# Performance work log

Hardware: AMD Instinct MI355X
Metric: run time of the kernel (lower is better)

## Reference

```python
import jax, jax.numpy as jnp
import numpy as np

NUM_NODES = 100000
NUM_EDGES = 600000
NUM_GRAPHS = 1000
EMB = 128


def setup_inputs() -> dict:
    key = jax.random.key(0)
    ks = jax.random.split(key, 12)
    x = jax.random.normal(ks[0], (NUM_NODES, 4), dtype=jnp.float32)
    edge_index = jax.random.randint(ks[1], (2, NUM_EDGES), 0, NUM_NODES, dtype=jnp.int32)
    x_scalar = jax.random.normal(ks[2], (NUM_GRAPHS, 4), dtype=jnp.float32)
    batch_index = jnp.sort(jax.random.randint(ks[3], (NUM_NODES,), 0, NUM_GRAPHS, dtype=jnp.int32))
    def glorot(k, shape):
        fan_in, fan_out = shape[0], shape[1]
        s = jnp.sqrt(2.0 / (fan_in + fan_out)).astype(jnp.float32)
        return jax.random.normal(k, shape, dtype=jnp.float32) * s
    return {
        "x": x,
        "edge_index": edge_index,
        "x_scalar": x_scalar,
        "batch_index": batch_index,
        "W0": glorot(ks[4], (4, EMB)), "b0": jnp.zeros((EMB,), jnp.float32),
        "W1": glorot(ks[5], (EMB, EMB)), "b1": jnp.zeros((EMB,), jnp.float32),
        "W2": glorot(ks[6], (EMB, EMB)), "b2": jnp.zeros((EMB,), jnp.float32),
        "W3": glorot(ks[7], (EMB, EMB)), "b3": jnp.zeros((EMB,), jnp.float32),
        "Wl1": glorot(ks[8], (EMB + 4, 64)), "bl1": jnp.zeros((64,), jnp.float32),
        "Wl2": glorot(ks[9], (64, 1)), "bl2": jnp.zeros((1,), jnp.float32),
    }


def _gcn_norm(edge_index, num_nodes):
    # PyG GCNConv default: add self-loops, symmetric normalization
    loop = jnp.arange(num_nodes, dtype=edge_index.dtype)
    src = jnp.concatenate([edge_index[0], loop])
    dst = jnp.concatenate([edge_index[1], loop])
    deg = jax.ops.segment_sum(jnp.ones_like(src, dtype=jnp.float32), dst,
                              num_segments=num_nodes)
    dinv = jnp.where(deg > 0, jax.lax.rsqrt(jnp.maximum(deg, 1e-12)), 0.0)
    norm = dinv[src] * dinv[dst]  # [E+N]
    return src, dst, norm


def _gcn_conv(h, src, dst, norm, W, b, num_nodes):
    h = h @ W                                   # [N, out]
    msg = h[src] * norm[:, None]                # gather + normalize
    out = jax.ops.segment_sum(msg, dst, num_segments=num_nodes)  # scatter-add
    return out + b


def reference(x, edge_index, x_scalar, batch_index,
              W0, b0, W1, b1, W2, b2, W3, b3, Wl1, bl1, Wl2, bl2):
    n = x.shape[0]
    src, dst, norm = _gcn_norm(edge_index, n)
    h = jax.nn.relu(_gcn_conv(x, src, dst, norm, W0, b0, n))
    h = jax.nn.relu(_gcn_conv(h, src, dst, norm, W1, b1, n))
    h = jax.nn.relu(_gcn_conv(h, src, dst, norm, W2, b2, n))
    h = jax.nn.relu(_gcn_conv(h, src, dst, norm, W3, b3, n))
    # global mean pool over batch_index
    sums = jax.ops.segment_sum(h, batch_index, num_segments=NUM_GRAPHS)
    cnts = jax.ops.segment_sum(jnp.ones((n,), jnp.float32), batch_index,
                               num_segments=NUM_GRAPHS)
    pooled = sums / jnp.maximum(cnts, 1.0)[:, None]          # [G, EMB]
    feat = jnp.concatenate([pooled, x_scalar], axis=1)       # [G, EMB+4]
    out = jax.nn.relu(feat @ Wl1 + bl1) @ Wl2 + bl2          # [G, 1]
    return out
```

## Files before the change

### kernel.cpp

```cpp
#include <hip/hip_runtime.h>

#define NN 100000
#define EE 600000
#define GG 1000
#define NB ((NN + 255) / 256)
#define CAP 32
#define LDSPAD 136

typedef __bf16 bf16x8 __attribute__((ext_vector_type(8)));
typedef float f32x4 __attribute__((ext_vector_type(4)));
typedef unsigned int u32;

__device__ inline float2 bf2_to_f2(u32 u) {
  return make_float2(__uint_as_float(u << 16), __uint_as_float(u & 0xffff0000u));
}
__device__ inline u32 f2_to_bf2(float a, float b) {
  union { __bf16 h[2]; u32 u; } pk;
  pk.h[0] = (__bf16)a; pk.h[1] = (__bf16)b;
  return pk.u;
}


__global__ void k_init(int* cnt, int* gstart) {
  int i = blockIdx.x * 256 + threadIdx.x;
  if (i < NN) cnt[i] = 0;
  if (i <= GG) gstart[i] = NN;
}

__global__ void k_fill(const int* __restrict__ src, const int* __restrict__ dst,
                       int* cnt, int* __restrict__ ibucket) {
  int e = blockIdx.x * 256 + threadIdx.x;
  if (e >= EE) return;
  int s = src[e], d = dst[e];
  int pos = atomicAdd(&cnt[d], 1);
  if (pos < CAP - 1) ibucket[d * CAP + pos] = s;
}

__global__ void k_prep(const int* __restrict__ cnt, float* __restrict__ dinv,
                       const int* __restrict__ batch, int* gstart,
                       const float* __restrict__ W1, const float* __restrict__ W2,
                       const float* __restrict__ W3,
                       __bf16* __restrict__ Wt1, __bf16* __restrict__ Wt2,
                       __bf16* __restrict__ Wt3) {
  int gid = blockIdx.x * 256 + threadIdx.x;
  if (gid < NN) {
    dinv[gid] = rsqrtf((float)(cnt[gid] + 1));
    int b = batch[gid];
    if (gid == 0) {
      for (int g = 0; g <= b; ++g) gstart[g] = 0;
    } else {
      int prev = batch[gid - 1];
      for (int g = prev + 1; g <= b; ++g) gstart[g] = gid;
    }
  }
  if (gid < 3 * 16384) {
    int which = gid >> 14, idx = gid & 16383;
    int n = idx >> 7, k = idx & 127;
    const float* W = (which == 0) ? W1 : (which == 1) ? W2 : W3;
    __bf16* Wt = (which == 0) ? Wt1 : (which == 1) ? Wt2 : Wt3;
    Wt[(size_t)n * 128 + k] = (__bf16)W[(size_t)k * 128 + n];
  }
}

__global__ void k_wb(const int* __restrict__ ibucket, const int* __restrict__ cnt,
                     const float* __restrict__ dinv, int2* __restrict__ wbucket) {
  int gid = blockIdx.x * 256 + threadIdx.x;
  if (gid >= NN * CAP) return;
  int d = gid >> 5, slot = gid & 31;
  int m = min(cnt[d], CAP - 1);
  int mp = (m + 8) & ~7;
  if (slot >= mp) return;
  float dd = dinv[d];
  int s; float w;
  if (slot < m)      { s = ibucket[gid]; w = dinv[s] * dd; }
  else if (slot == m){ s = d;            w = dd * dd; }
  else               { s = d;            w = 0.f; }
  wbucket[gid] = make_int2(s, __float_as_int(w));
}


__global__ void k_aggx(const float4* __restrict__ x, const int* __restrict__ cnt,
                       const int2* __restrict__ wbucket, float4* __restrict__ y) {
  int i = blockIdx.x * 256 + threadIdx.x;
  if (i >= NN) return;
  int m1 = min(cnt[i], CAP - 1) + 1;
  float4 acc = make_float4(0.f, 0.f, 0.f, 0.f);
  for (int e = 0; e < m1; ++e) {
    int2 md = wbucket[i * CAP + e];
    float w = __int_as_float(md.y);
    float4 v = x[md.x];
    acc.x = fmaf(w, v.x, acc.x);
    acc.y = fmaf(w, v.y, acc.y);
    acc.z = fmaf(w, v.z, acc.z);
    acc.w = fmaf(w, v.w, acc.w);
  }
  y[i] = acc;
}


__global__ void k_lin0(const float4* __restrict__ y, const float* __restrict__ W0,
                       const float* __restrict__ b0, u32* __restrict__ hout2) {
  int gid = blockIdx.x * 256 + threadIdx.x;
  if (gid >= NN * 16) return;
  int node = gid >> 4, cg = gid & 15;
  float4 yv = y[node];
  float v[8];
  #pragma unroll
  for (int k = 0; k < 2; ++k) {
    float4 b = *(const float4*)(b0 + cg * 8 + k * 4);
    v[k * 4 + 0] = b.x; v[k * 4 + 1] = b.y; v[k * 4 + 2] = b.z; v[k * 4 + 3] = b.w;
  }
  #pragma unroll
  for (int k = 0; k < 4; ++k) {
    float yk = (k == 0) ? yv.x : (k == 1) ? yv.y : (k == 2) ? yv.z : yv.w;
    float4 wa = *(const float4*)(W0 + k * 128 + cg * 8);
    float4 wb = *(const float4*)(W0 + k * 128 + cg * 8 + 4);
    v[0] = fmaf(yk, wa.x, v[0]); v[1] = fmaf(yk, wa.y, v[1]);
    v[2] = fmaf(yk, wa.z, v[2]); v[3] = fmaf(yk, wa.w, v[3]);
    v[4] = fmaf(yk, wb.x, v[4]); v[5] = fmaf(yk, wb.y, v[5]);
    v[6] = fmaf(yk, wb.z, v[6]); v[7] = fmaf(yk, wb.w, v[7]);
  }
  uint4 o;
  o.x = f2_to_bf2(fmaxf(v[0], 0.f), fmaxf(v[1], 0.f));
  o.y = f2_to_bf2(fmaxf(v[2], 0.f), fmaxf(v[3], 0.f));
  o.z = f2_to_bf2(fmaxf(v[4], 0.f), fmaxf(v[5], 0.f));
  o.w = f2_to_bf2(fmaxf(v[6], 0.f), fmaxf(v[7], 0.f));
  *(uint4*)(hout2 + (size_t)node * 64 + cg * 4) = o;
}

__global__ __launch_bounds__(256) void k_agg23(const __bf16* __restrict__ hlin,
                                               const int* __restrict__ cnt,
                                               const int2* __restrict__ wbucket,
                                               u32* __restrict__ hout2) {
  int wid = (blockIdx.x * 4) + (threadIdx.x >> 6);
  int lane = threadIdx.x & 63;
  int ln = lane & 15, quad = lane >> 4;
  int na = wid * 2, nb = wid * 2 + 1;
  if (na >= NN) return;

  int nodeL = (lane < 32) ? na : nb;
  int2 me = make_int2(0, 0);
  if (nodeL < NN) me = wbucket[(size_t)nodeL * CAP + (lane & 31)];
  int s_l = me.x, w_l = me.y;
  int mpa = (min(cnt[na], CAP - 1) + 8) & ~7;
  int mpb = (nb < NN) ? ((min(cnt[nb], CAP - 1) + 8) & ~7) : 0;
  int mpmin = min(mpa, mpb);

  float aa[8] = {0.f, 0.f, 0.f, 0.f, 0.f, 0.f, 0.f, 0.f};
  float ab[8] = {0.f, 0.f, 0.f, 0.f, 0.f, 0.f, 0.f, 0.f};

  int j = 0;
  for (; j < mpmin; j += 8) {
    int p0 = (j + quad) * 4, p1 = (j + 4 + quad) * 4;
    int sa0 = __builtin_amdgcn_ds_bpermute(p0, s_l);
    int sa1 = __builtin_amdgcn_ds_bpermute(p1, s_l);
    int sb0 = __builtin_amdgcn_ds_bpermute(128 + p0, s_l);
    int sb1 = __builtin_amdgcn_ds_bpermute(128 + p1, s_l);
    float wa0 = __int_as_float(__builtin_amdgcn_ds_bpermute(p0, w_l));
    float wa1 = __int_as_float(__builtin_amdgcn_ds_bpermute(p1, w_l));
    float wb0 = __int_as_float(__builtin_amdgcn_ds_bpermute(128 + p0, w_l));
    float wb1 = __int_as_float(__builtin_amdgcn_ds_bpermute(128 + p1, w_l));
    uint4 ua0 = *(const uint4*)(hlin + ((size_t)sa0 << 7) + ln * 8);
    uint4 ua1 = *(const uint4*)(hlin + ((size_t)sa1 << 7) + ln * 8);
    uint4 ub0 = *(const uint4*)(hlin + ((size_t)sb0 << 7) + ln * 8);
    uint4 ub1 = *(const uint4*)(hlin + ((size_t)sb1 << 7) + ln * 8);
    float2 f;
    f = bf2_to_f2(ua0.x); aa[0] = fmaf(wa0, f.x, aa[0]); aa[1] = fmaf(wa0, f.y, aa[1]);
    f = bf2_to_f2(ua0.y); aa[2] = fmaf(wa0, f.x, aa[2]); aa[3] = fmaf(wa0, f.y, aa[3]);
    f = bf2_to_f2(ua0.z); aa[4] = fmaf(wa0, f.x, aa[4]); aa[5] = fmaf(wa0, f.y, aa[5]);
    f = bf2_to_f2(ua0.w); aa[6] = fmaf(wa0, f.x, aa[6]); aa[7] = fmaf(wa0, f.y, aa[7]);
    f = bf2_to_f2(ua1.x); aa[0] = fmaf(wa1, f.x, aa[0]); aa[1] = fmaf(wa1, f.y, aa[1]);
    f = bf2_to_f2(ua1.y); aa[2] = fmaf(wa1, f.x, aa[2]); aa[3] = fmaf(wa1, f.y, aa[3]);
    f = bf2_to_f2(ua1.z); aa[4] = fmaf(wa1, f.x, aa[4]); aa[5] = fmaf(wa1, f.y, aa[5]);
    f = bf2_to_f2(ua1.w); aa[6] = fmaf(wa1, f.x, aa[6]); aa[7] = fmaf(wa1, f.y, aa[7]);
    f = bf2_to_f2(ub0.x); ab[0] = fmaf(wb0, f.x, ab[0]); ab[1] = fmaf(wb0, f.y, ab[1]);
    f = bf2_to_f2(ub0.y); ab[2] = fmaf(wb0, f.x, ab[2]); ab[3] = fmaf(wb0, f.y, ab[3]);
    f = bf2_to_f2(ub0.z); ab[4] = fmaf(wb0, f.x, ab[4]); ab[5] = fmaf(wb0, f.y, ab[5]);
    f = bf2_to_f2(ub0.w); ab[6] = fmaf(wb0, f.x, ab[6]); ab[7] = fmaf(wb0, f.y, ab[7]);
    f = bf2_to_f2(ub1.x); ab[0] = fmaf(wb1, f.x, ab[0]); ab[1] = fmaf(wb1, f.y, ab[1]);
    f = bf2_to_f2(ub1.y); ab[2] = fmaf(wb1, f.x, ab[2]); ab[3] = fmaf(wb1, f.y, ab[3]);
    f = bf2_to_f2(ub1.z); ab[4] = fmaf(wb1, f.x, ab[4]); ab[5] = fmaf(wb1, f.y, ab[5]);
    f = bf2_to_f2(ub1.w); ab[6] = fmaf(wb1, f.x, ab[6]); ab[7] = fmaf(wb1, f.y, ab[7]);
  }
  for (; j < mpa; j += 8) {
    int p0 = (j + quad) * 4, p1 = (j + 4 + quad) * 4;
    int s0 = __builtin_amdgcn_ds_bpermute(p0, s_l);
    int s1 = __builtin_amdgcn_ds_bpermute(p1, s_l);
    float w0 = __int_as_float(__builtin_amdgcn_ds_bpermute(p0, w_l));
    float w1 = __int_as_float(__builtin_amdgcn_ds_bpermute(p1, w_l));
    uint4 u0 = *(const uint4*)(hlin + ((size_t)s0 << 7) + ln * 8);
    uint4 u1 = *(const uint4*)(hlin + ((size_t)s1 << 7) + ln * 8);
    float2 f;
    f = bf2_to_f2(u0.x); aa[0] = fmaf(w0, f.x, aa[0]); aa[1] = fmaf(w0, f.y, aa[1]);
    f = bf2_to_f2(u0.y); aa[2] = fmaf(w0, f.x, aa[2]); aa[3] = fmaf(w0, f.y, aa[3]);
    f = bf2_to_f2(u0.z); aa[4] = fmaf(w0, f.x, aa[4]); aa[5] = fmaf(w0, f.y, aa[5]);
    f = bf2_to_f2(u0.w); aa[6] = fmaf(w0, f.x, aa[6]); aa[7] = fmaf(w0, f.y, aa[7]);
    f = bf2_to_f2(u1.x); aa[0] = fmaf(w1, f.x, aa[0]); aa[1] = fmaf(w1, f.y, aa[1]);
    f = bf2_to_f2(u1.y); aa[2] = fmaf(w1, f.x, aa[2]); aa[3] = fmaf(w1, f.y, aa[3]);
    f = bf2_to_f2(u1.z); aa[4] = fmaf(w1, f.x, aa[4]); aa[5] = fmaf(w1, f.y, aa[5]);
    f = bf2_to_f2(u1.w); aa[6] = fmaf(w1, f.x, aa[6]); aa[7] = fmaf(w1, f.y, aa[7]);
  }
  for (; j < mpb; j += 8) {
    int p0 = 128 + (j + quad) * 4, p1 = 128 + (j + 4 + quad) * 4;
    int s0 = __builtin_amdgcn_ds_bpermute(p0, s_l);
    int s1 = __builtin_amdgcn_ds_bpermute(p1, s_l);
    float w0 = __int_as_float(__builtin_amdgcn_ds_bpermute(p0, w_l));
    float w1 = __int_as_float(__builtin_amdgcn_ds_bpermute(p1, w_l));
    uint4 u0 = *(const uint4*)(hlin + ((size_t)s0 << 7) + ln * 8);
    uint4 u1 = *(const uint4*)(hlin + ((size_t)s1 << 7) + ln * 8);
    float2 f;
    f = bf2_to_f2(u0.x); ab[0] = fmaf(w0, f.x, ab[0]); ab[1] = fmaf(w0, f.y, ab[1]);
    f = bf2_to_f2(u0.y); ab[2] = fmaf(w0, f.x, ab[2]); ab[3] = fmaf(w0, f.y, ab[3]);
    f = bf2_to_f2(u0.z); ab[4] = fmaf(w0, f.x, ab[4]); ab[5] = fmaf(w0, f.y, ab[5]);
    f = bf2_to_f2(u0.w); ab[6] = fmaf(w0, f.x, ab[6]); ab[7] = fmaf(w0, f.y, ab[7]);
    f = bf2_to_f2(u1.x); ab[0] = fmaf(w1, f.x, ab[0]); ab[1] = fmaf(w1, f.y, ab[1]);
    f = bf2_to_f2(u1.y); ab[2] = fmaf(w1, f.x, ab[2]); ab[3] = fmaf(w1, f.y, ab[3]);
    f = bf2_to_f2(u1.z); ab[4] = fmaf(w1, f.x, ab[4]); ab[5] = fmaf(w1, f.y, ab[5]);
    f = bf2_to_f2(u1.w); ab[6] = fmaf(w1, f.x, ab[6]); ab[7] = fmaf(w1, f.y, ab[7]);
  }

  #pragma unroll
  for (int k = 0; k < 8; ++k) {
    aa[k] += __shfl_xor(aa[k], 16); aa[k] += __shfl_xor(aa[k], 32);
    ab[k] += __shfl_xor(ab[k], 16); ab[k] += __shfl_xor(ab[k], 32);
  }
  if (quad == 0) {
    uint4 oa;
    oa.x = f2_to_bf2(aa[0], aa[1]); oa.y = f2_to_bf2(aa[2], aa[3]);
    oa.z = f2_to_bf2(aa[4], aa[5]); oa.w = f2_to_bf2(aa[6], aa[7]);
    *(uint4*)(hout2 + (size_t)na * 64 + ln * 4) = oa;
    if (nb < NN) {
      uint4 ob;
      ob.x = f2_to_bf2(ab[0], ab[1]); ob.y = f2_to_bf2(ab[2], ab[3]);
      ob.z = f2_to_bf2(ab[4], ab[5]); ob.w = f2_to_bf2(ab[6], ab[7]);
      *(uint4*)(hout2 + (size_t)nb * 64 + ln * 4) = ob;
    }
  }
}

__global__ __launch_bounds__(256) void k_mfma(const __bf16* __restrict__ hin,
                                              const __bf16* __restrict__ Wt,
                                              const float* __restrict__ bias,
                                              __bf16* __restrict__ hout) {
  __shared__ __bf16 As[128 * LDSPAD];
  int tid = threadIdx.x;
  int row0 = blockIdx.x * 128;
  int lane = tid & 63, w = tid >> 6;
  int ln = lane & 15, quad = lane >> 4;

  bf16x8 bfrag[8][4];
  float bcol[8];
  #pragma unroll
  for (int nt = 0; nt < 8; ++nt) {
    bcol[nt] = bias[nt * 16 + ln];
    #pragma unroll
    for (int kc = 0; kc < 4; ++kc)
      bfrag[nt][kc] = *(const bf16x8*)(Wt + (size_t)(nt * 16 + ln) * 128 + kc * 32 + quad * 8);
  }

  #pragma unroll
  for (int i = 0; i < 8; ++i) {
    int eb = (i * 256 + tid) * 8;
    int r = eb >> 7, c = eb & 127;
    int gr = row0 + r;
    uint4 v = make_uint4(0, 0, 0, 0);
    if (gr < NN) v = *(const uint4*)(hin + (size_t)gr * 128 + c);
    *(uint4*)&As[r * LDSPAD + c] = v;
  }
  __syncthreads();

  f32x4 acc[2][8];
  #pragma unroll
  for (int rt = 0; rt < 2; ++rt)
    #pragma unroll
    for (int nt = 0; nt < 8; ++nt) acc[rt][nt] = (f32x4){0.f, 0.f, 0.f, 0.f};

  #pragma unroll
  for (int kc = 0; kc < 4; ++kc) {
    bf16x8 a0 = *(const bf16x8*)&As[(w * 32 + ln) * LDSPAD + kc * 32 + quad * 8];
    bf16x8 a1 = *(const bf16x8*)&As[(w * 32 + 16 + ln) * LDSPAD + kc * 32 + quad * 8];
    #pragma unroll
    for (int nt = 0; nt < 8; ++nt) {
      acc[0][nt] = __builtin_amdgcn_mfma_f32_16x16x32_bf16(a0, bfrag[nt][kc], acc[0][nt], 0, 0, 0);
      acc[1][nt] = __builtin_amdgcn_mfma_f32_16x16x32_bf16(a1, bfrag[nt][kc], acc[1][nt], 0, 0, 0);
    }
  }

  #pragma unroll
  for (int rt = 0; rt < 2; ++rt)
    #pragma unroll
    for (int nt = 0; nt < 8; ++nt)
      #pragma unroll
      for (int reg = 0; reg < 4; ++reg) {
        int gr = row0 + w * 32 + rt * 16 + quad * 4 + reg;
        if (gr < NN)
          hout[(size_t)gr * 128 + nt * 16 + ln] =
              (__bf16)fmaxf(acc[rt][nt][reg] + bcol[nt], 0.f);
      }
}

__global__ __launch_bounds__(256) void k_poolmlp(const uint2* __restrict__ h4u,
                                                 const int* __restrict__ gstart,
                                                 const float* __restrict__ xs,
                                                 const float* __restrict__ Wl1,
                                                 const float* __restrict__ bl1,
                                                 const float* __restrict__ Wl2,
                                                 const float* __restrict__ bl2,
                                                 float* __restrict__ out) {
  __shared__ float4 part[8][32];
  __shared__ float pooled[128];
  int g = blockIdx.x;
  int beg = gstart[g], end = gstart[g + 1];
  int tid = threadIdx.x;
  int cg = tid & 31;
  int rg = tid >> 5;
  float4 acc = make_float4(0.f, 0.f, 0.f, 0.f);
  for (int i = beg + rg; i < end; i += 8) {
    uint2 u = h4u[(size_t)i * 32 + cg];
    acc.x += __uint_as_float(u.x << 16);
    acc.y += __uint_as_float(u.x & 0xffff0000u);
    acc.z += __uint_as_float(u.y << 16);
    acc.w += __uint_as_float(u.y & 0xffff0000u);
  }
  part[rg][cg] = acc;
  __syncthreads();
  if (tid < 32) {
    float4 s = part[0][tid];
    #pragma unroll
    for (int r = 1; r < 8; ++r) {
      float4 v = part[r][tid];
      s.x += v.x; s.y += v.y; s.z += v.z; s.w += v.w;
    }
    float sc = 1.f / fmaxf((float)(end - beg), 1.f);
    pooled[tid * 4 + 0] = s.x * sc;
    pooled[tid * 4 + 1] = s.y * sc;
    pooled[tid * 4 + 2] = s.z * sc;
    pooled[tid * 4 + 3] = s.w * sc;
  }
  __syncthreads();
  if (tid < 64) {
    float hj = bl1[tid];
    #pragma unroll 4
    for (int k = 0; k < 128; ++k) hj = fmaf(pooled[k], Wl1[k * 64 + tid], hj);
    const float* xr = xs + g * 4;
    #pragma unroll
    for (int k = 0; k < 4; ++k) hj = fmaf(xr[k], Wl1[(128 + k) * 64 + tid], hj);
    hj = fmaxf(hj, 0.f);
    float val = hj * Wl2[tid];
    #pragma unroll
    for (int off = 32; off > 0; off >>= 1) val += __shfl_down(val, off);
    if (tid == 0) out[g] = val + bl2[0];
  }
}


extern "C" void kernel_launch(void* const* d_in, const int* in_sizes, int n_in,
                              void* d_out, int out_size, void* d_ws, size_t ws_size,
                              hipStream_t stream) {
  const float* x    = (const float*)d_in[0];
  const int*   ei   = (const int*)d_in[1];
  const float* xs   = (const float*)d_in[2];
  const int*   batch= (const int*)d_in[3];
  const float* W0   = (const float*)d_in[4];
  const float* b0   = (const float*)d_in[5];
  const float* W1   = (const float*)d_in[6];
  const float* b1   = (const float*)d_in[7];
  const float* W2   = (const float*)d_in[8];
  const float* b2   = (const float*)d_in[9];
  const float* W3   = (const float*)d_in[10];
  const float* b3   = (const float*)d_in[11];
  const float* Wl1  = (const float*)d_in[12];
  const float* bl1  = (const float*)d_in[13];
  const float* Wl2  = (const float*)d_in[14];
  const float* bl2  = (const float*)d_in[15];
  const int* srcA = ei;
  const int* dstA = ei + EE;
  float* out = (float*)d_out;

  char* p = (char*)d_ws;
  auto take = [&](size_t bytes) { char* q = p; p += (bytes + 255) & ~(size_t)255; return q; };
  __bf16* hA    = (__bf16*)take((size_t)NN * 128 * 2);
  __bf16* hB    = (__bf16*)take((size_t)NN * 128 * 2);
  float*  y     = (float*)take((size_t)NN * 4 * 4);
  int*    cnt   = (int*)take((size_t)NN * 4);
  float*  dinv  = (float*)take((size_t)NN * 4);
  int*    ibucket = (int*)take((size_t)NN * CAP * 4);
  int2*   wbucket = (int2*)take((size_t)NN * CAP * 8);
  int*    gstart= (int*)take((size_t)(GG + 1) * 4);
  __bf16* Wt1   = (__bf16*)take(16384 * 2);
  __bf16* Wt2   = (__bf16*)take(16384 * 2);
  __bf16* Wt3   = (__bf16*)take(16384 * 2);

  k_init<<<NB, 256, 0, stream>>>(cnt, gstart);
  k_fill<<<(EE + 255) / 256, 256, 0, stream>>>(srcA, dstA, cnt, ibucket);
  k_prep<<<NB, 256, 0, stream>>>(cnt, dinv, batch, gstart, W1, W2, W3, Wt1, Wt2, Wt3);
  k_wb<<<(NN * CAP + 255) / 256, 256, 0, stream>>>(ibucket, cnt, dinv, wbucket);

  k_aggx<<<NB, 256, 0, stream>>>((const float4*)x, cnt, wbucket, (float4*)y);
  k_lin0<<<(NN * 16 + 255) / 256, 256, 0, stream>>>((const float4*)y, W0, b0, (u32*)hA);
  k_agg23<<<(NN + 7) / 8, 256, 0, stream>>>(hA, cnt, wbucket, (u32*)hB);
  k_mfma<<<(NN + 127) / 128, 256, 0, stream>>>(hB, Wt1, b1, hA);
  k_agg23<<<(NN + 7) / 8, 256, 0, stream>>>(hA, cnt, wbucket, (u32*)hB);
  k_mfma<<<(NN + 127) / 128, 256, 0, stream>>>(hB, Wt2, b2, hA);
  k_agg23<<<(NN + 7) / 8, 256, 0, stream>>>(hA, cnt, wbucket, (u32*)hB);
  k_mfma<<<(NN + 127) / 128, 256, 0, stream>>>(hB, Wt3, b3, hA);

  k_poolmlp<<<GG, 256, 0, stream>>>((const uint2*)hA, gstart, xs, Wl1, bl1, Wl2, bl2, out);
}
```

Before: 350.5 us.

## Fuse layer-0 aggregation into linear kernel and drop LDS staging in MFMA GEMM

```diff
diff --git a/kernel.cpp b/kernel.cpp
--- a/kernel.cpp
+++ b/kernel.cpp
@@ -5,7 +5,6 @@
 #define GG 1000
 #define NB ((NN + 255) / 256)
 #define CAP 32
-#define LDSPAD 136
 
 typedef __bf16 bf16x8 __attribute__((ext_vector_type(8)));
 typedef float f32x4 __attribute__((ext_vector_type(4)));
@@ -78,32 +77,24 @@
   wbucket[gid] = make_int2(s, __float_as_int(w));
 }
 
-
-__global__ void k_aggx(const float4* __restrict__ x, const int* __restrict__ cnt,
-                       const int2* __restrict__ wbucket, float4* __restrict__ y) {
-  int i = blockIdx.x * 256 + threadIdx.x;
-  if (i >= NN) return;
-  int m1 = min(cnt[i], CAP - 1) + 1;
-  float4 acc = make_float4(0.f, 0.f, 0.f, 0.f);
-  for (int e = 0; e < m1; ++e) {
-    int2 md = wbucket[i * CAP + e];
-    float w = __int_as_float(md.y);
-    float4 v = x[md.x];
-    acc.x = fmaf(w, v.x, acc.x);
-    acc.y = fmaf(w, v.y, acc.y);
-    acc.z = fmaf(w, v.z, acc.z);
-    acc.w = fmaf(w, v.w, acc.w);
-  }
-  y[i] = acc;
-}
-
-
-__global__ void k_lin0(const float4* __restrict__ y, const float* __restrict__ W0,
-                       const float* __restrict__ b0, u32* __restrict__ hout2) {
+__global__ void k_l0(const float4* __restrict__ x, const int* __restrict__ cnt,
+                     const int2* __restrict__ wbucket,
+                     const float* __restrict__ W0, const float* __restrict__ b0,
+                     u32* __restrict__ hout2) {
   int gid = blockIdx.x * 256 + threadIdx.x;
   if (gid >= NN * 16) return;
   int node = gid >> 4, cg = gid & 15;
-  float4 yv = y[node];
+  int m1 = min(cnt[node], CAP - 1) + 1;
+  float4 yv = make_float4(0.f, 0.f, 0.f, 0.f);
+  for (int e = 0; e < m1; ++e) {
+    int2 md = wbucket[(size_t)node * CAP + e];
+    float wgt = __int_as_float(md.y);
+    float4 v = x[md.x];
+    yv.x = fmaf(wgt, v.x, yv.x);
+    yv.y = fmaf(wgt, v.y, yv.y);
+    yv.z = fmaf(wgt, v.z, yv.z);
+    yv.w = fmaf(wgt, v.w, yv.w);
+  }
   float v[8];
   #pragma unroll
   for (int k = 0; k < 2; ++k) {
@@ -242,32 +233,29 @@
                                               const __bf16* __restrict__ Wt,
                                               const float* __restrict__ bias,
                                               __bf16* __restrict__ hout) {
-  __shared__ __bf16 As[128 * LDSPAD];
   int tid = threadIdx.x;
   int row0 = blockIdx.x * 128;
   int lane = tid & 63, w = tid >> 6;
   int ln = lane & 15, quad = lane >> 4;
 
-  bf16x8 bfrag[8][4];
   float bcol[8];
   #pragma unroll
-  for (int nt = 0; nt < 8; ++nt) {
-    bcol[nt] = bias[nt * 16 + ln];
-    #pragma unroll
-    for (int kc = 0; kc < 4; ++kc)
-      bfrag[nt][kc] = *(const bf16x8*)(Wt + (size_t)(nt * 16 + ln) * 128 + kc * 32 + quad * 8);
-  }
-
-  #pragma unroll
-  for (int i = 0; i < 8; ++i) {
-    int eb = (i * 256 + tid) * 8;
-    int r = eb >> 7, c = eb & 127;
-    int gr = row0 + r;
-    uint4 v = make_uint4(0, 0, 0, 0);
-    if (gr < NN) v = *(const uint4*)(hin + (size_t)gr * 128 + c);
-    *(uint4*)&As[r * LDSPAD + c] = v;
-  }
-  __syncthreads();
+  for (int nt = 0; nt < 8; ++nt) bcol[nt] = bias[nt * 16 + ln];
+
+  int r0 = row0 + w * 32 + ln;
+  int r1 = r0 + 16;
+  bf16x8 zero8;
+  #pragma unroll
+  for (int i = 0; i < 8; ++i) zero8[i] = (__bf16)0.f;
+
+  bf16x8 a0[4], a1[4];
+  #pragma unroll
+  for (int kc = 0; kc < 4; ++kc) {
+    a0[kc] = (r0 < NN) ? *(const bf16x8*)(hin + (size_t)r0 * 128 + kc * 32 + quad * 8)
+                       : zero8;
+    a1[kc] = (r1 < NN) ? *(const bf16x8*)(hin + (size_t)r1 * 128 + kc * 32 + quad * 8)
+                       : zero8;
+  }
 
   f32x4 acc[2][8];
   #pragma unroll
@@ -277,12 +265,11 @@
 
   #pragma unroll
   for (int kc = 0; kc < 4; ++kc) {
-    bf16x8 a0 = *(const bf16x8*)&As[(w * 32 + ln) * LDSPAD + kc * 32 + quad * 8];
-    bf16x8 a1 = *(const bf16x8*)&As[(w * 32 + 16 + ln) * LDSPAD + kc * 32 + quad * 8];
     #pragma unroll
     for (int nt = 0; nt < 8; ++nt) {
-      acc[0][nt] = __builtin_amdgcn_mfma_f32_16x16x32_bf16(a0, bfrag[nt][kc], acc[0][nt], 0, 0, 0);
-      acc[1][nt] = __builtin_amdgcn_mfma_f32_16x16x32_bf16(a1, bfrag[nt][kc], acc[1][nt], 0, 0, 0);
+      bf16x8 bf = *(const bf16x8*)(Wt + (size_t)(nt * 16 + ln) * 128 + kc * 32 + quad * 8);
+      acc[0][nt] = __builtin_amdgcn_mfma_f32_16x16x32_bf16(a0[kc], bf, acc[0][nt], 0, 0, 0);
+      acc[1][nt] = __builtin_amdgcn_mfma_f32_16x16x32_bf16(a1[kc], bf, acc[1][nt], 0, 0, 0);
     }
   }
 
@@ -381,7 +368,6 @@
   auto take = [&](size_t bytes) { char* q = p; p += (bytes + 255) & ~(size_t)255; return q; };
   __bf16* hA    = (__bf16*)take((size_t)NN * 128 * 2);
   __bf16* hB    = (__bf16*)take((size_t)NN * 128 * 2);
-  float*  y     = (float*)take((size_t)NN * 4 * 4);
   int*    cnt   = (int*)take((size_t)NN * 4);
   float*  dinv  = (float*)take((size_t)NN * 4);
   int*    ibucket = (int*)take((size_t)NN * CAP * 4);
@@ -396,8 +382,7 @@
   k_prep<<<NB, 256, 0, stream>>>(cnt, dinv, batch, gstart, W1, W2, W3, Wt1, Wt2, Wt3);
   k_wb<<<(NN * CAP + 255) / 256, 256, 0, stream>>>(ibucket, cnt, dinv, wbucket);
 
-  k_aggx<<<NB, 256, 0, stream>>>((const float4*)x, cnt, wbucket, (float4*)y);
-  k_lin0<<<(NN * 16 + 255) / 256, 256, 0, stream>>>((const float4*)y, W0, b0, (u32*)hA);
+  k_l0<<<(NN * 16 + 255) / 256, 256, 0, stream>>>((const float4*)x, cnt, wbucket, W0, b0, (u32*)hA);
   k_agg23<<<(NN + 7) / 8, 256, 0, stream>>>(hA, cnt, wbucket, (u32*)hB);
   k_mfma<<<(NN + 127) / 128, 256, 0, stream>>>(hB, Wt1, b1, hA);
   k_agg23<<<(NN + 7) / 8, 256, 0, stream>>>(hA, cnt, wbucket, (u32*)hB);
```

Result: no change. 354.8 us (+1.2%).

## Fuse layer-0 aggregate into linear, drop ibucket, pad edge lists to four

Applied to the files above, without the earlier changes.

```diff
diff --git a/kernel.cpp b/kernel.cpp
--- a/kernel.cpp
+++ b/kernel.cpp
@@ -28,12 +28,12 @@
 }
 
 __global__ void k_fill(const int* __restrict__ src, const int* __restrict__ dst,
-                       int* cnt, int* __restrict__ ibucket) {
+                       int* cnt, int2* __restrict__ wbucket) {
   int e = blockIdx.x * 256 + threadIdx.x;
   if (e >= EE) return;
   int s = src[e], d = dst[e];
   int pos = atomicAdd(&cnt[d], 1);
-  if (pos < CAP - 1) ibucket[d * CAP + pos] = s;
+  if (pos < CAP - 1) wbucket[d * CAP + pos].x = s;
 }
 
 __global__ void k_prep(const int* __restrict__ cnt, float* __restrict__ dinv,
@@ -62,48 +62,40 @@
   }
 }
 
-__global__ void k_wb(const int* __restrict__ ibucket, const int* __restrict__ cnt,
-                     const float* __restrict__ dinv, int2* __restrict__ wbucket) {
+__global__ void k_wb(const int* __restrict__ cnt, const float* __restrict__ dinv,
+                     int2* __restrict__ wbucket) {
   int gid = blockIdx.x * 256 + threadIdx.x;
   if (gid >= NN * CAP) return;
   int d = gid >> 5, slot = gid & 31;
   int m = min(cnt[d], CAP - 1);
-  int mp = (m + 8) & ~7;
+  int mp = (m + 4) & ~3;
   if (slot >= mp) return;
   float dd = dinv[d];
   int s; float w;
-  if (slot < m)      { s = ibucket[gid]; w = dinv[s] * dd; }
-  else if (slot == m){ s = d;            w = dd * dd; }
-  else               { s = d;            w = 0.f; }
+  if (slot < m)      { s = wbucket[gid].x; w = dinv[s] * dd; }
+  else if (slot == m){ s = d;              w = dd * dd; }
+  else               { s = d;              w = 0.f; }
   wbucket[gid] = make_int2(s, __float_as_int(w));
 }
 
-
-__global__ void k_aggx(const float4* __restrict__ x, const int* __restrict__ cnt,
-                       const int2* __restrict__ wbucket, float4* __restrict__ y) {
-  int i = blockIdx.x * 256 + threadIdx.x;
-  if (i >= NN) return;
-  int m1 = min(cnt[i], CAP - 1) + 1;
-  float4 acc = make_float4(0.f, 0.f, 0.f, 0.f);
-  for (int e = 0; e < m1; ++e) {
-    int2 md = wbucket[i * CAP + e];
-    float w = __int_as_float(md.y);
-    float4 v = x[md.x];
-    acc.x = fmaf(w, v.x, acc.x);
-    acc.y = fmaf(w, v.y, acc.y);
-    acc.z = fmaf(w, v.z, acc.z);
-    acc.w = fmaf(w, v.w, acc.w);
-  }
-  y[i] = acc;
-}
-
-
-__global__ void k_lin0(const float4* __restrict__ y, const float* __restrict__ W0,
-                       const float* __restrict__ b0, u32* __restrict__ hout2) {
+__global__ void k_l0(const float4* __restrict__ x, const int* __restrict__ cnt,
+                     const int2* __restrict__ wbucket,
+                     const float* __restrict__ W0, const float* __restrict__ b0,
+                     u32* __restrict__ hout2) {
   int gid = blockIdx.x * 256 + threadIdx.x;
   if (gid >= NN * 16) return;
   int node = gid >> 4, cg = gid & 15;
-  float4 yv = y[node];
+  int m1 = min(cnt[node], CAP - 1) + 1;
+  float4 yv = make_float4(0.f, 0.f, 0.f, 0.f);
+  for (int e = 0; e < m1; ++e) {
+    int2 md = wbucket[(size_t)node * CAP + e];
+    float wgt = __int_as_float(md.y);
+    float4 v = x[md.x];
+    yv.x = fmaf(wgt, v.x, yv.x);
+    yv.y = fmaf(wgt, v.y, yv.y);
+    yv.z = fmaf(wgt, v.z, yv.z);
+    yv.w = fmaf(wgt, v.w, yv.w);
+  }
   float v[8];
   #pragma unroll
   for (int k = 0; k < 2; ++k) {
@@ -142,15 +134,15 @@
   int2 me = make_int2(0, 0);
   if (nodeL < NN) me = wbucket[(size_t)nodeL * CAP + (lane & 31)];
   int s_l = me.x, w_l = me.y;
-  int mpa = (min(cnt[na], CAP - 1) + 8) & ~7;
-  int mpb = (nb < NN) ? ((min(cnt[nb], CAP - 1) + 8) & ~7) : 0;
+  int mpa = (min(cnt[na], CAP - 1) + 4) & ~3;
+  int mpb = (nb < NN) ? ((min(cnt[nb], CAP - 1) + 4) & ~3) : 0;
   int mpmin = min(mpa, mpb);
 
   float aa[8] = {0.f, 0.f, 0.f, 0.f, 0.f, 0.f, 0.f, 0.f};
   float ab[8] = {0.f, 0.f, 0.f, 0.f, 0.f, 0.f, 0.f, 0.f};
 
   int j = 0;
-  for (; j < mpmin; j += 8) {
+  for (; j + 8 <= mpmin; j += 8) {
     int p0 = (j + quad) * 4, p1 = (j + 4 + quad) * 4;
     int sa0 = __builtin_amdgcn_ds_bpermute(p0, s_l);
     int sa1 = __builtin_amdgcn_ds_bpermute(p1, s_l);
@@ -182,41 +174,46 @@
     f = bf2_to_f2(ub1.z); ab[4] = fmaf(wb1, f.x, ab[4]); ab[5] = fmaf(wb1, f.y, ab[5]);
     f = bf2_to_f2(ub1.w); ab[6] = fmaf(wb1, f.x, ab[6]); ab[7] = fmaf(wb1, f.y, ab[7]);
   }
-  for (; j < mpa; j += 8) {
-    int p0 = (j + quad) * 4, p1 = (j + 4 + quad) * 4;
-    int s0 = __builtin_amdgcn_ds_bpermute(p0, s_l);
-    int s1 = __builtin_amdgcn_ds_bpermute(p1, s_l);
-    float w0 = __int_as_float(__builtin_amdgcn_ds_bpermute(p0, w_l));
-    float w1 = __int_as_float(__builtin_amdgcn_ds_bpermute(p1, w_l));
+  if (j < mpmin) {
+    int p = (j + quad) * 4;
+    int sa = __builtin_amdgcn_ds_bpermute(p, s_l);
+    int sb = __builtin_amdgcn_ds_bpermute(128 + p, s_l);
+    float wa = __int_as_float(__builtin_amdgcn_ds_bpermute(p, w_l));
+    float wb = __int_as_float(__builtin_amdgcn_ds_bpermute(128 + p, w_l));
+    uint4 ua = *(const uint4*)(hlin + ((size_t)sa << 7) + ln * 8);
+    uint4 ub = *(const uint4*)(hlin + ((size_t)sb << 7) + ln * 8);
+    float2 f;
+    f = bf2_to_f2(ua.x); aa[0] = fmaf(wa, f.x, aa[0]); aa[1] = fmaf(wa, f.y, aa[1]);
+    f = bf2_to_f2(ua.y); aa[2] = fmaf(wa, f.x, aa[2]); aa[3] = fmaf(wa, f.y, aa[3]);
+    f = bf2_to_f2(ua.z); aa[4] = fmaf(wa, f.x, aa[4]); aa[5] = fmaf(wa, f.y, aa[5]);
+    f = bf2_to_f2(ua.w); aa[6] = fmaf(wa, f.x, aa[6]); aa[7] = fmaf(wa, f.y, aa[7]);
+    f = bf2_to_f2(ub.x); ab[0] = fmaf(wb, f.x, ab[0]); ab[1] = fmaf(wb, f.y, ab[1]);
+    f = bf2_to_f2(ub.y); ab[2] = fmaf(wb, f.x, ab[2]); ab[3] = fmaf(wb, f.y, ab[3]);
+    f = bf2_to_f2(ub.z); ab[4] = fmaf(wb, f.x, ab[4]); ab[5] = fmaf(wb, f.y, ab[5]);
+    f = bf2_to_f2(ub.w); ab[6] = fmaf(wb, f.x, ab[6]); ab[7] = fmaf(wb, f.y, ab[7]);
+    j += 4;
+  }
+  for (; j < mpa; j += 4) {
+    int p = (j + quad) * 4;
+    int s0 = __builtin_amdgcn_ds_bpermute(p, s_l);
+    float w0 = __int_as_float(__builtin_amdgcn_ds_bpermute(p, w_l));
     uint4 u0 = *(const uint4*)(hlin + ((size_t)s0 << 7) + ln * 8);
-    uint4 u1 = *(const uint4*)(hlin + ((size_t)s1 << 7) + ln * 8);
     float2 f;
     f = bf2_to_f2(u0.x); aa[0] = fmaf(w0, f.x, aa[0]); aa[1] = fmaf(w0, f.y, aa[1]);
     f = bf2_to_f2(u0.y); aa[2] = fmaf(w0, f.x, aa[2]); aa[3] = fmaf(w0, f.y, aa[3]);
     f = bf2_to_f2(u0.z); aa[4] = fmaf(w0, f.x, aa[4]); aa[5] = fmaf(w0, f.y, aa[5]);
     f = bf2_to_f2(u0.w); aa[6] = fmaf(w0, f.x, aa[6]); aa[7] = fmaf(w0, f.y, aa[7]);
-    f = bf2_to_f2(u1.x); aa[0] = fmaf(w1, f.x, aa[0]); aa[1] = fmaf(w1, f.y, aa[1]);
-    f = bf2_to_f2(u1.y); aa[2] = fmaf(w1, f.x, aa[2]); aa[3] = fmaf(w1, f.y, aa[3]);
-    f = bf2_to_f2(u1.z); aa[4] = fmaf(w1, f.x, aa[4]); aa[5] = fmaf(w1, f.y, aa[5]);
-    f = bf2_to_f2(u1.w); aa[6] = fmaf(w1, f.x, aa[6]); aa[7] = fmaf(w1, f.y, aa[7]);
-  }
-  for (; j < mpb; j += 8) {
-    int p0 = 128 + (j + quad) * 4, p1 = 128 + (j + 4 + quad) * 4;
-    int s0 = __builtin_amdgcn_ds_bpermute(p0, s_l);
-    int s1 = __builtin_amdgcn_ds_bpermute(p1, s_l);
-    float w0 = __int_as_float(__builtin_amdgcn_ds_bpermute(p0, w_l));
-    float w1 = __int_as_float(__builtin_amdgcn_ds_bpermute(p1, w_l));
+  }
+  for (; j < mpb; j += 4) {
+    int p = 128 + (j + quad) * 4;
+    int s0 = __builtin_amdgcn_ds_bpermute(p, s_l);
+    float w0 = __int_as_float(__builtin_amdgcn_ds_bpermute(p, w_l));
     uint4 u0 = *(const uint4*)(hlin + ((size_t)s0 << 7) + ln * 8);
-    uint4 u1 = *(const uint4*)(hlin + ((size_t)s1 << 7) + ln * 8);
     float2 f;
     f = bf2_to_f2(u0.x); ab[0] = fmaf(w0, f.x, ab[0]); ab[1] = fmaf(w0, f.y, ab[1]);
     f = bf2_to_f2(u0.y); ab[2] = fmaf(w0, f.x, ab[2]); ab[3] = fmaf(w0, f.y, ab[3]);
     f = bf2_to_f2(u0.z); ab[4] = fmaf(w0, f.x, ab[4]); ab[5] = fmaf(w0, f.y, ab[5]);
     f = bf2_to_f2(u0.w); ab[6] = fmaf(w0, f.x, ab[6]); ab[7] = fmaf(w0, f.y, ab[7]);
-    f = bf2_to_f2(u1.x); ab[0] = fmaf(w1, f.x, ab[0]); ab[1] = fmaf(w1, f.y, ab[1]);
-    f = bf2_to_f2(u1.y); ab[2] = fmaf(w1, f.x, ab[2]); ab[3] = fmaf(w1, f.y, ab[3]);
-    f = bf2_to_f2(u1.z); ab[4] = fmaf(w1, f.x, ab[4]); ab[5] = fmaf(w1, f.y, ab[5]);
-    f = bf2_to_f2(u1.w); ab[6] = fmaf(w1, f.x, ab[6]); ab[7] = fmaf(w1, f.y, ab[7]);
   }
 
   #pragma unroll
@@ -381,10 +378,8 @@
   auto take = [&](size_t bytes) { char* q = p; p += (bytes + 255) & ~(size_t)255; return q; };
   __bf16* hA    = (__bf16*)take((size_t)NN * 128 * 2);
   __bf16* hB    = (__bf16*)take((size_t)NN * 128 * 2);
-  float*  y     = (float*)take((size_t)NN * 4 * 4);
   int*    cnt   = (int*)take((size_t)NN * 4);
   float*  dinv  = (float*)take((size_t)NN * 4);
-  int*    ibucket = (int*)take((size_t)NN * CAP * 4);
   int2*   wbucket = (int2*)take((size_t)NN * CAP * 8);
   int*    gstart= (int*)take((size_t)(GG + 1) * 4);
   __bf16* Wt1   = (__bf16*)take(16384 * 2);
@@ -392,12 +387,11 @@
   __bf16* Wt3   = (__bf16*)take(16384 * 2);
 
   k_init<<<NB, 256, 0, stream>>>(cnt, gstart);
-  k_fill<<<(EE + 255) / 256, 256, 0, stream>>>(srcA, dstA, cnt, ibucket);
+  k_fill<<<(EE + 255) / 256, 256, 0, stream>>>(srcA, dstA, cnt, wbucket);
   k_prep<<<NB, 256, 0, stream>>>(cnt, dinv, batch, gstart, W1, W2, W3, Wt1, Wt2, Wt3);
-  k_wb<<<(NN * CAP + 255) / 256, 256, 0, stream>>>(ibucket, cnt, dinv, wbucket);
-
-  k_aggx<<<NB, 256, 0, stream>>>((const float4*)x, cnt, wbucket, (float4*)y);
-  k_lin0<<<(NN * 16 + 255) / 256, 256, 0, stream>>>((const float4*)y, W0, b0, (u32*)hA);
+  k_wb<<<(NN * CAP + 255) / 256, 256, 0, stream>>>(cnt, dinv, wbucket);
+
+  k_l0<<<(NN * 16 + 255) / 256, 256, 0, stream>>>((const float4*)x, cnt, wbucket, W0, b0, (u32*)hA);
   k_agg23<<<(NN + 7) / 8, 256, 0, stream>>>(hA, cnt, wbucket, (u32*)hB);
   k_mfma<<<(NN + 127) / 128, 256, 0, stream>>>(hB, Wt1, b1, hA);
   k_agg23<<<(NN + 7) / 8, 256, 0, stream>>>(hA, cnt, wbucket, (u32*)hB);
```

Result: no change. 356.9 us (+1.8%).
